# Optimization experiments

Measured on AMD Instinct MI355X. Metric: run time of the kernel, lower is better.

## Reference

```python
import jax, jax.numpy as jnp
import numpy as np

NUM_USERS = 100000
NUM_ITEMS = 50000
EMBED_DIM = 64
N_NODES = NUM_USERS + NUM_ITEMS
N_EDGES = 4800000
N_LAYERS = 3


def setup_inputs() -> dict:
    key = jax.random.key(0)
    k = jax.random.split(key, 7)
    return {
        "users": jax.random.randint(k[0], (16384,), 0, NUM_USERS),
        "items": jax.random.randint(k[1], (16384,), 0, NUM_ITEMS),
        "user_emb": jax.random.normal(k[2], (NUM_USERS, EMBED_DIM), dtype=jnp.float32) * 0.1,
        "item_emb": jax.random.normal(k[3], (NUM_ITEMS, EMBED_DIM), dtype=jnp.float32) * 0.1,
        "adj_rows": jax.random.randint(k[4], (N_EDGES,), 0, N_NODES),
        "adj_cols": jax.random.randint(k[5], (N_EDGES,), 0, N_NODES),
        "adj_vals": jax.random.uniform(k[6], (N_EDGES,), dtype=jnp.float32) * (1.0 / 32.0),
    }


def _spmm(rows, cols, vals, x):
    # y[r] = sum_{e: rows[e]==r} vals[e] * x[cols[e]]   (COO SpMM)
    msgs = vals[:, None] * x[cols]              # [nnz, d]
    return jax.ops.segment_sum(msgs, rows, num_segments=N_NODES)


def reference(users, items, user_emb, item_emb, adj_rows, adj_cols, adj_vals):
    ego = jnp.concatenate([user_emb, item_emb], axis=0)   # [N, d]
    acc = ego                                             # running sum of layer outputs
    h = ego
    for _ in range(N_LAYERS):
        h = _spmm(adj_rows, adj_cols, adj_vals, h)
        acc = acc + h
    final = acc / jnp.asarray(N_LAYERS + 1, dtype=acc.dtype)  # mean over layers
    final_users = final[:NUM_USERS]
    final_items = final[NUM_USERS:]
    u = final_users[users]                                # [B, d]
    v = final_items[items]                                # [B, d]
    return jnp.sum(u * v, axis=1)                         # [B]
```

## Files before the change

### kernel.cpp

```cpp
#include <hip/hip_runtime.h>

#define NUM_USERS 100000
#define NUM_ITEMS 50000
#define EMBED_DIM 64
#define N_NODES   (NUM_USERS + NUM_ITEMS)
#define N_EDGES   4800000
#define N_QUERY   16384

#define NODE_FLOATS ((size_t)N_NODES * EMBED_DIM)
#define NODE_FLOAT4 (NODE_FLOATS / 4)
#define SCAN_BLOCKS ((N_NODES + 255) / 256)

#define NBUCKET    256
#define BROWS      586
#define BUCKET_CAP 20480
#define BIN_EDGES  8192
#define BIN_THREADS 512
#define BIN_BLOCKS ((N_EDGES + BIN_EDGES - 1) / BIN_EDGES)

__device__ __forceinline__ float4 bf2f4(uint2 u) {
    float4 f;
    f.x = __uint_as_float(u.x << 16);
    f.y = __uint_as_float(u.x & 0xFFFF0000u);
    f.z = __uint_as_float(u.y << 16);
    f.w = __uint_as_float(u.y & 0xFFFF0000u);
    return f;
}
__device__ __forceinline__ unsigned rne_bf(float f) {
    unsigned b = __float_as_uint(f);
    return (b + 0x7FFFu + ((b >> 16) & 1u)) >> 16;
}
__device__ __forceinline__ uint2 f42bf(float4 f) {
    uint2 u;
    u.x = rne_bf(f.x) | (rne_bf(f.y) << 16);
    u.y = rne_bf(f.z) | (rne_bf(f.w) << 16);
    return u;
}
__device__ __forceinline__ void fma4v(float v, float4 xv, float4& av) {
    av.x = fmaf(v, xv.x, av.x);
    av.y = fmaf(v, xv.y, av.y);
    av.z = fmaf(v, xv.z, av.z);
    av.w = fmaf(v, xv.w, av.w);
}

__global__ void ego_bf_kernel(const float4* __restrict__ ue4,
                              const float4* __restrict__ ie4,
                              uint2* __restrict__ ego) {
    size_t i = (size_t)blockIdx.x * blockDim.x + threadIdx.x;
    if (i >= NODE_FLOAT4) return;
    const size_t user_f4 = (size_t)NUM_USERS * EMBED_DIM / 4;
    float4 v = (i < user_f4) ? ue4[i] : ie4[i - user_f4];
    ego[i] = f42bf(v);
}

__global__ void flag_kernel(const int* __restrict__ users,
                            const int* __restrict__ items,
                            int* __restrict__ flag,
                            int* __restrict__ gcur) {
    int i = blockIdx.x * blockDim.x + threadIdx.x;
    if (blockIdx.x == 0 && threadIdx.x < NBUCKET)
        gcur[threadIdx.x] = threadIdx.x * BUCKET_CAP;
    if (i < N_QUERY) {
        flag[users[i]] = 1;
        flag[NUM_USERS + items[i]] = 1;
    }
}

__global__ void compact_kernel(const int* __restrict__ flag,
                               int* __restrict__ qlist,
                               int* __restrict__ qn) {
    int i = blockIdx.x * blockDim.x + threadIdx.x;
    if (i < N_NODES && flag[i])
        qlist[atomicAdd(qn, 1)] = i;
}

__global__ void __launch_bounds__(BIN_THREADS) bin_kernel(
        const int* __restrict__ rows,
        const int* __restrict__ cols,
        const float* __restrict__ vals,
        int* __restrict__ gcur,
        int2* __restrict__ rec) {
    __shared__ int  lcnt[NBUCKET];
    __shared__ int  lbase[NBUCKET];
    __shared__ int  loff[NBUCKET];
    __shared__ int  lcur[NBUCKET];
    __shared__ int  scan[NBUCKET];
    __shared__ int2 sRec[BIN_EDGES];

    const int tid = threadIdx.x;
    if (tid < NBUCKET) lcnt[tid] = 0;
    __syncthreads();

    const size_t e0 = (size_t)blockIdx.x * BIN_EDGES;

    for (int k = tid; k < BIN_EDGES; k += BIN_THREADS) {
        size_t e = e0 + k;
        if (e < N_EDGES)
            atomicAdd(&lcnt[rows[e] / BROWS], 1);
    }
    __syncthreads();

    if (tid < NBUCKET) {
        lbase[tid] = atomicAdd(&gcur[tid], lcnt[tid]);
        scan[tid]  = lcnt[tid];
    }
    __syncthreads();
    for (int off = 1; off < NBUCKET; off <<= 1) {
        int tv = (tid < NBUCKET && tid >= off) ? scan[tid - off] : 0;
        __syncthreads();
        if (tid < NBUCKET) scan[tid] += tv;
        __syncthreads();
    }
    if (tid < NBUCKET) {
        loff[tid] = scan[tid] - lcnt[tid];
        lcur[tid] = loff[tid];
    }
    __syncthreads();

    for (int k = tid; k < BIN_EDGES; k += BIN_THREADS) {
        size_t e = e0 + k;
        if (e < N_EDGES) {
            int r  = rows[e];
            int b  = r / BROWS;
            int rl = r - b * BROWS;
            int slot = atomicAdd(&lcur[b], 1);
            sRec[slot] = make_int2((rl << 18) | cols[e], __float_as_int(vals[e]));
        }
    }
    __syncthreads();

    int wv = tid >> 6, ln = tid & 63;
    for (int b = wv; b < NBUCKET; b += (BIN_THREADS / 64)) {
        int n = lcnt[b], src = loff[b], dst = lbase[b];
        for (int k = ln; k < n; k += 64)
            rec[(size_t)dst + k] = sRec[src + k];
    }
}

__global__ void __launch_bounds__(256) csr_kernel(
        const int2* __restrict__ rec,
        const int* __restrict__ gcur,
        int* __restrict__ row_start,
        int* __restrict__ row_cnt,
        int2* __restrict__ pair) {
    __shared__ int hist[BROWS + 2];
    __shared__ int excl[768];
    __shared__ int part[256];

    const int b    = blockIdx.x;
    const int base = b * BUCKET_CAP;
    const int n    = gcur[b] - base;
    const int lo   = b * BROWS;
    const int t    = threadIdx.x;

    for (int j = t; j < BROWS; j += 256) hist[j] = 0;
    __syncthreads();

    for (int i = t; i < n; i += 256)
        atomicAdd(&hist[rec[base + i].x >> 18], 1);
    __syncthreads();

    int vloc[3];
    int s0 = 0;
    #pragma unroll
    for (int k = 0; k < 3; ++k) {
        int idx = t * 3 + k;
        int v = (idx < BROWS) ? hist[idx] : 0;
        vloc[k] = s0;
        s0 += v;
    }
    part[t] = s0;
    __syncthreads();
    for (int off = 1; off < 256; off <<= 1) {
        int tv = (t >= off) ? part[t - off] : 0;
        __syncthreads();
        part[t] += tv;
        __syncthreads();
    }
    int pbase = part[t] - s0;
    #pragma unroll
    for (int k = 0; k < 3; ++k) {
        int idx = t * 3 + k;
        if (idx < BROWS) excl[idx] = pbase + vloc[k];
    }
    __syncthreads();

    for (int j = t; j < BROWS; j += 256) {
        row_start[lo + j] = base + excl[j];
        row_cnt[lo + j]   = hist[j];
    }
    __syncthreads();

    for (int i = t; i < n; i += 256) {
        int2 p = rec[base + i];
        int rl = p.x >> 18;
        int slot = atomicAdd(&excl[rl], 1);
        pair[(size_t)base + slot] = make_int2(p.x & 0x3FFFF, p.y);
    }
}

__device__ __forceinline__ float4 gather_row(int s, int e, int g, int q,
                                             const int2* __restrict__ pair,
                                             const uint2* __restrict__ hb) {
    float4 av = make_float4(0.f, 0.f, 0.f, 0.f);
    int i = s;
    for (; i + 16 <= e; i += 16) {
        int2 p0 = pair[i + g];
        int2 p1 = pair[i + 4 + g];
        int2 p2 = pair[i + 8 + g];
        int2 p3 = pair[i + 12 + g];
        uint2 u0 = hb[(size_t)p0.x * 16 + q];
        uint2 u1 = hb[(size_t)p1.x * 16 + q];
        uint2 u2 = hb[(size_t)p2.x * 16 + q];
        uint2 u3 = hb[(size_t)p3.x * 16 + q];
        fma4v(__int_as_float(p0.y), bf2f4(u0), av);
        fma4v(__int_as_float(p1.y), bf2f4(u1), av);
        fma4v(__int_as_float(p2.y), bf2f4(u2), av);
        fma4v(__int_as_float(p3.y), bf2f4(u3), av);
    }
    if (i + 8 <= e) {
        int2 p0 = pair[i + g];
        int2 p1 = pair[i + 4 + g];
        uint2 u0 = hb[(size_t)p0.x * 16 + q];
        uint2 u1 = hb[(size_t)p1.x * 16 + q];
        fma4v(__int_as_float(p0.y), bf2f4(u0), av);
        fma4v(__int_as_float(p1.y), bf2f4(u1), av);
        i += 8;
    }
    if (i + 4 <= e) {
        int2 p0 = pair[i + g];
        uint2 u0 = hb[(size_t)p0.x * 16 + q];
        fma4v(__int_as_float(p0.y), bf2f4(u0), av);
        i += 4;
    }
    if (i < e) {
        int idx = i + g;
        int2 pD = pair[(idx < e) ? idx : (e - 1)];
        float vD = (idx < e) ? __int_as_float(pD.y) : 0.0f;
        uint2 uD = hb[(size_t)pD.x * 16 + q];
        fma4v(vD, bf2f4(uD), av);
    }
    av.x += __shfl_xor(av.x, 32, 64);
    av.y += __shfl_xor(av.y, 32, 64);
    av.z += __shfl_xor(av.z, 32, 64);
    av.w += __shfl_xor(av.w, 32, 64);
    av.x += __shfl_xor(av.x, 16, 64);
    av.y += __shfl_xor(av.y, 16, 64);
    av.z += __shfl_xor(av.z, 16, 64);
    av.w += __shfl_xor(av.w, 16, 64);
    return av;
}

__global__ void spmm_kernel(const int* __restrict__ row_start,
                            const int* __restrict__ row_cnt,
                            const int2* __restrict__ pair,
                            const uint2* __restrict__ hb,
                            uint2* __restrict__ hn) {
    int wid  = (int)(((size_t)blockIdx.x * blockDim.x + threadIdx.x) >> 6);
    int lane = threadIdx.x & 63;
    int g = lane >> 4, q = lane & 15;
    if (wid >= N_NODES) return;
    int s = row_start[wid];
    int e = s + row_cnt[wid];

    float4 av = gather_row(s, e, g, q, pair, hb);

    if (lane < 16)
        hn[(size_t)wid * 16 + q] = f42bf(av);
}

__global__ void final_kernel(const int* __restrict__ row_start,
                             const int* __restrict__ row_cnt,
                             const int2* __restrict__ pair,
                             const uint2* __restrict__ hB,
                             const uint2* __restrict__ hA,
                             const float4* __restrict__ ue4,
                             const float4* __restrict__ ie4,
                             float4* __restrict__ fin4,
                             const int* __restrict__ qlist,
                             const int* __restrict__ qn) {
    int wid  = (int)(((size_t)blockIdx.x * blockDim.x + threadIdx.x) >> 6);
    int lane = threadIdx.x & 63;
    int g = lane >> 4, q = lane & 15;
    if (wid >= *qn) return;
    int row = qlist[wid];
    int s = row_start[row];
    int e = s + row_cnt[row];

    float4 av = gather_row(s, e, g, q, pair, hB);

    if (lane < 16) {
        size_t o = (size_t)row * 16 + q;
        float4 ego = (row < NUM_USERS)
                   ? ue4[(size_t)row * 16 + q]
                   : ie4[(size_t)(row - NUM_USERS) * 16 + q];
        float4 a1 = bf2f4(hA[o]);
        float4 a2 = bf2f4(hB[o]);
        float4 f;
        f.x = 0.25f * (ego.x + a1.x + a2.x + av.x);
        f.y = 0.25f * (ego.y + a1.y + a2.y + av.y);
        f.z = 0.25f * (ego.z + a1.z + a2.z + av.z);
        f.w = 0.25f * (ego.w + a1.w + a2.w + av.w);
        fin4[o] = f;
    }
}

__global__ void dot_kernel(const int* __restrict__ users,
                           const int* __restrict__ items,
                           const float* __restrict__ fin,
                           float* __restrict__ out) {
    int lane = threadIdx.x & 63;
    int wave = threadIdx.x >> 6;
    int q    = blockIdx.x * (blockDim.x >> 6) + wave;
    if (q >= N_QUERY) return;

    float a = fin[(size_t)users[q] * EMBED_DIM + lane];
    float b = fin[((size_t)NUM_USERS + items[q]) * EMBED_DIM + lane];
    float p = a * b;

    #pragma unroll
    for (int off = 32; off >= 1; off >>= 1)
        p += __shfl_xor(p, off, 64);

    if (lane == 0)
        out[q] = p;
}

extern "C" void kernel_launch(void* const* d_in, const int* in_sizes, int n_in,
                              void* d_out, int out_size, void* d_ws, size_t ws_size,
                              hipStream_t stream) {
    const int*   users = (const int*)  d_in[0];
    const int*   items = (const int*)  d_in[1];
    const float* ue    = (const float*)d_in[2];
    const float* ie    = (const float*)d_in[3];
    const int*   rows  = (const int*)  d_in[4];
    const int*   cols  = (const int*)  d_in[5];
    const float* vals  = (const float*)d_in[6];
    float*       out   = (float*)d_out;

    const size_t REC_N = (size_t)NBUCKET * BUCKET_CAP;

    float* fin    = (float*)d_ws;
    uint2* ego_bf = (uint2*)(fin + NODE_FLOATS);
    uint2* hA_bf  = ego_bf + NODE_FLOAT4;
    uint2* hB_bf  = hA_bf + NODE_FLOAT4;
    int2*  rec    = (int2*)ego_bf;
    int2*  pair   = (int2*)(hB_bf + NODE_FLOAT4);

    int* row_start = (int*)(pair + REC_N);
    int* row_cnt   = row_start + 150016;
    int* flag      = row_cnt + 150016;
    int* qn        = flag + N_NODES;
    int* gcur      = qn + 1;
    int* qlist     = gcur + NBUCKET;

    int vec_blocks = (int)((NODE_FLOAT4 + 255) / 256);

    (void)hipMemsetAsync(flag, 0, (size_t)(N_NODES + 1) * sizeof(int), stream);

    flag_kernel<<<(N_QUERY + 255) / 256, 256, 0, stream>>>(users, items, flag, gcur);

    bin_kernel<<<BIN_BLOCKS, BIN_THREADS, 0, stream>>>(rows, cols, vals, gcur, rec);
    csr_kernel<<<NBUCKET, 256, 0, stream>>>(rec, gcur, row_start, row_cnt, pair);

    ego_bf_kernel<<<vec_blocks, 256, 0, stream>>>(
        (const float4*)ue, (const float4*)ie, ego_bf);

    int spmm_blocks = (N_NODES * 64 + 255) / 256;
    spmm_kernel<<<spmm_blocks, 256, 0, stream>>>(row_start, row_cnt, pair, ego_bf, hA_bf);
    spmm_kernel<<<spmm_blocks, 256, 0, stream>>>(row_start, row_cnt, pair, hA_bf, hB_bf);

    compact_kernel<<<SCAN_BLOCKS, 256, 0, stream>>>(flag, qlist, qn);

    int q_blocks = (2 * N_QUERY * 64 + 255) / 256;
    final_kernel<<<q_blocks, 256, 0, stream>>>(row_start, row_cnt, pair,
        hB_bf, hA_bf, (const float4*)ue, (const float4*)ie, (float4*)fin, qlist, qn);

    dot_kernel<<<(N_QUERY + 3) / 4, 256, 0, stream>>>(users, items, fin, out);
}
```

Before: 364.6 us.

## Pad CSR rows to even offsets for int4 pair loads; drop query dedup

Row segments in the CSR pair array now start at even offsets, because each row's size is rounded up to an even count in the prefix scan. This lets the gather loop fetch two (col,val) pairs per int4 load and process 32 edges per iteration. The flag, memset and compact passes are removed, and the final kernel now processes every user and item query directly, duplicates included. The cost is padding slack in each bucket and redundant final-layer gathers for repeated query nodes. The padding also leaves unwritten pair slots, but the loop bounds appear to exclude them.

```diff
diff --git a/kernel.cpp b/kernel.cpp
--- a/kernel.cpp
+++ b/kernel.cpp
@@ -9,7 +9,6 @@
 
 #define NODE_FLOATS ((size_t)N_NODES * EMBED_DIM)
 #define NODE_FLOAT4 (NODE_FLOATS / 4)
-#define SCAN_BLOCKS ((N_NODES + 255) / 256)
 
 #define NBUCKET    256
 #define BROWS      586
@@ -41,6 +40,11 @@
     av.y = fmaf(v, xv.y, av.y);
     av.z = fmaf(v, xv.z, av.z);
     av.w = fmaf(v, xv.w, av.w);
+}
+
+__global__ void init_gcur_kernel(int* __restrict__ gcur) {
+    if (threadIdx.x < NBUCKET)
+        gcur[threadIdx.x] = threadIdx.x * BUCKET_CAP;
 }
 
 __global__ void ego_bf_kernel(const float4* __restrict__ ue4,
@@ -51,27 +55,6 @@
     const size_t user_f4 = (size_t)NUM_USERS * EMBED_DIM / 4;
     float4 v = (i < user_f4) ? ue4[i] : ie4[i - user_f4];
     ego[i] = f42bf(v);
-}
-
-__global__ void flag_kernel(const int* __restrict__ users,
-                            const int* __restrict__ items,
-                            int* __restrict__ flag,
-                            int* __restrict__ gcur) {
-    int i = blockIdx.x * blockDim.x + threadIdx.x;
-    if (blockIdx.x == 0 && threadIdx.x < NBUCKET)
-        gcur[threadIdx.x] = threadIdx.x * BUCKET_CAP;
-    if (i < N_QUERY) {
-        flag[users[i]] = 1;
-        flag[NUM_USERS + items[i]] = 1;
-    }
-}
-
-__global__ void compact_kernel(const int* __restrict__ flag,
-                               int* __restrict__ qlist,
-                               int* __restrict__ qn) {
-    int i = blockIdx.x * blockDim.x + threadIdx.x;
-    if (i < N_NODES && flag[i])
-        qlist[atomicAdd(qn, 1)] = i;
 }
 
 __global__ void __launch_bounds__(BIN_THREADS) bin_kernel(
@@ -165,7 +148,7 @@
     #pragma unroll
     for (int k = 0; k < 3; ++k) {
         int idx = t * 3 + k;
-        int v = (idx < BROWS) ? hist[idx] : 0;
+        int v = (idx < BROWS) ? ((hist[idx] + 1) & ~1) : 0;
         vloc[k] = s0;
         s0 += v;
     }
@@ -204,27 +187,47 @@
                                              const uint2* __restrict__ hb) {
     float4 av = make_float4(0.f, 0.f, 0.f, 0.f);
     int i = s;
-    for (; i + 16 <= e; i += 16) {
-        int2 p0 = pair[i + g];
-        int2 p1 = pair[i + 4 + g];
-        int2 p2 = pair[i + 8 + g];
-        int2 p3 = pair[i + 12 + g];
-        uint2 u0 = hb[(size_t)p0.x * 16 + q];
-        uint2 u1 = hb[(size_t)p1.x * 16 + q];
-        uint2 u2 = hb[(size_t)p2.x * 16 + q];
-        uint2 u3 = hb[(size_t)p3.x * 16 + q];
-        fma4v(__int_as_float(p0.y), bf2f4(u0), av);
-        fma4v(__int_as_float(p1.y), bf2f4(u1), av);
-        fma4v(__int_as_float(p2.y), bf2f4(u2), av);
-        fma4v(__int_as_float(p3.y), bf2f4(u3), av);
+    for (; i + 32 <= e; i += 32) {
+        int4 pp0 = *(const int4*)(pair + i      + 2*g);
+        int4 pp1 = *(const int4*)(pair + i +  8 + 2*g);
+        int4 pp2 = *(const int4*)(pair + i + 16 + 2*g);
+        int4 pp3 = *(const int4*)(pair + i + 24 + 2*g);
+        uint2 u0 = hb[(size_t)pp0.x * 16 + q];
+        uint2 u1 = hb[(size_t)pp0.z * 16 + q];
+        uint2 u2 = hb[(size_t)pp1.x * 16 + q];
+        uint2 u3 = hb[(size_t)pp1.z * 16 + q];
+        uint2 u4 = hb[(size_t)pp2.x * 16 + q];
+        uint2 u5 = hb[(size_t)pp2.z * 16 + q];
+        uint2 u6 = hb[(size_t)pp3.x * 16 + q];
+        uint2 u7 = hb[(size_t)pp3.z * 16 + q];
+        fma4v(__int_as_float(pp0.y), bf2f4(u0), av);
+        fma4v(__int_as_float(pp0.w), bf2f4(u1), av);
+        fma4v(__int_as_float(pp1.y), bf2f4(u2), av);
+        fma4v(__int_as_float(pp1.w), bf2f4(u3), av);
+        fma4v(__int_as_float(pp2.y), bf2f4(u4), av);
+        fma4v(__int_as_float(pp2.w), bf2f4(u5), av);
+        fma4v(__int_as_float(pp3.y), bf2f4(u6), av);
+        fma4v(__int_as_float(pp3.w), bf2f4(u7), av);
+    }
+    if (i + 16 <= e) {
+        int4 pp0 = *(const int4*)(pair + i     + 2*g);
+        int4 pp1 = *(const int4*)(pair + i + 8 + 2*g);
+        uint2 u0 = hb[(size_t)pp0.x * 16 + q];
+        uint2 u1 = hb[(size_t)pp0.z * 16 + q];
+        uint2 u2 = hb[(size_t)pp1.x * 16 + q];
+        uint2 u3 = hb[(size_t)pp1.z * 16 + q];
+        fma4v(__int_as_float(pp0.y), bf2f4(u0), av);
+        fma4v(__int_as_float(pp0.w), bf2f4(u1), av);
+        fma4v(__int_as_float(pp1.y), bf2f4(u2), av);
+        fma4v(__int_as_float(pp1.w), bf2f4(u3), av);
+        i += 16;
     }
     if (i + 8 <= e) {
-        int2 p0 = pair[i + g];
-        int2 p1 = pair[i + 4 + g];
-        uint2 u0 = hb[(size_t)p0.x * 16 + q];
-        uint2 u1 = hb[(size_t)p1.x * 16 + q];
-        fma4v(__int_as_float(p0.y), bf2f4(u0), av);
-        fma4v(__int_as_float(p1.y), bf2f4(u1), av);
+        int4 pp0 = *(const int4*)(pair + i + 2*g);
+        uint2 u0 = hb[(size_t)pp0.x * 16 + q];
+        uint2 u1 = hb[(size_t)pp0.z * 16 + q];
+        fma4v(__int_as_float(pp0.y), bf2f4(u0), av);
+        fma4v(__int_as_float(pp0.w), bf2f4(u1), av);
         i += 8;
     }
     if (i + 4 <= e) {
@@ -277,13 +280,13 @@
                              const float4* __restrict__ ue4,
                              const float4* __restrict__ ie4,
                              float4* __restrict__ fin4,
-                             const int* __restrict__ qlist,
-                             const int* __restrict__ qn) {
+                             const int* __restrict__ users,
+                             const int* __restrict__ items) {
     int wid  = (int)(((size_t)blockIdx.x * blockDim.x + threadIdx.x) >> 6);
     int lane = threadIdx.x & 63;
     int g = lane >> 4, q = lane & 15;
-    if (wid >= *qn) return;
-    int row = qlist[wid];
+    if (wid >= 2 * N_QUERY) return;
+    int row = (wid < N_QUERY) ? users[wid] : (NUM_USERS + items[wid - N_QUERY]);
     int s = row_start[row];
     int e = s + row_cnt[row];
 
@@ -349,17 +352,11 @@
 
     int* row_start = (int*)(pair + REC_N);
     int* row_cnt   = row_start + 150016;
-    int* flag      = row_cnt + 150016;
-    int* qn        = flag + N_NODES;
-    int* gcur      = qn + 1;
-    int* qlist     = gcur + NBUCKET;
+    int* gcur      = row_cnt + 150016;
 
     int vec_blocks = (int)((NODE_FLOAT4 + 255) / 256);
 
-    (void)hipMemsetAsync(flag, 0, (size_t)(N_NODES + 1) * sizeof(int), stream);
-
-    flag_kernel<<<(N_QUERY + 255) / 256, 256, 0, stream>>>(users, items, flag, gcur);
-
+    init_gcur_kernel<<<1, 256, 0, stream>>>(gcur);
     bin_kernel<<<BIN_BLOCKS, BIN_THREADS, 0, stream>>>(rows, cols, vals, gcur, rec);
     csr_kernel<<<NBUCKET, 256, 0, stream>>>(rec, gcur, row_start, row_cnt, pair);
 
@@ -370,11 +367,10 @@
     spmm_kernel<<<spmm_blocks, 256, 0, stream>>>(row_start, row_cnt, pair, ego_bf, hA_bf);
     spmm_kernel<<<spmm_blocks, 256, 0, stream>>>(row_start, row_cnt, pair, hA_bf, hB_bf);
 
-    compact_kernel<<<SCAN_BLOCKS, 256, 0, stream>>>(flag, qlist, qn);
-
     int q_blocks = (2 * N_QUERY * 64 + 255) / 256;
     final_kernel<<<q_blocks, 256, 0, stream>>>(row_start, row_cnt, pair,
-        hB_bf, hA_bf, (const float4*)ue, (const float4*)ie, (float4*)fin, qlist, qn);
+        hB_bf, hA_bf, (const float4*)ue, (const float4*)ie, (float4*)fin,
+        users, items);
 
     dot_kernel<<<(N_QUERY + 3) / 4, 256, 0, stream>>>(users, items, fin, out);
 }
```

Result: faster. 335.6 us (-8.0%).
